# Optimization experiments

Hardware: AMD Instinct MI355X
Metric: run time of the kernel (lower is better)

The kernel has to match this reference:

```python
import jax, jax.numpy as jnp
import numpy as np

B, L, SIZE, ATT, LIN = 8, 2048, 1024, 1024, 4096
EPS = 1e-5


def layer_norm(x, g, b):
    m = x.mean(-1, keepdims=True)
    v = ((x - m) ** 2).mean(-1, keepdims=True)
    return (x - m) * jax.lax.rsqrt(v + EPS) * g + b


def time_shift(x):
    # ZeroPad2d((0,0,1,-1)): prepend a zero timestep, drop the last one
    return jnp.pad(x, ((0, 0), (1, 0), (0, 0)))[:, :-1]


def wkv(time_decay, time_first, k, v):
    """RWKV-v4 WKV linear-attention recurrence (numerically stable, log-space max tracking).
    k, v: (B, L, D). Returns (B, L, D)."""
    w = -jnp.exp(time_decay)  # (D,) per-channel decay (negative)
    u = time_first            # (D,) bonus for current token

    def step(carry, kv):
        p, q, o = carry  # numerator, denominator, running max exponent: (B, D)
        kt, vt = kv      # (B, D)
        no = jnp.maximum(o, u + kt)
        A = jnp.exp(o - no)
        Bc = jnp.exp(u + kt - no)
        out = (A * p + Bc * vt) / (A * q + Bc)
        no2 = jnp.maximum(o + w, kt)
        A2 = jnp.exp(o + w - no2)
        B2 = jnp.exp(kt - no2)
        return (A2 * p + B2 * vt, A2 * q + B2, no2), out

    Bn, Ln, D = k.shape
    init = (jnp.zeros((Bn, D), k.dtype), jnp.zeros((Bn, D), k.dtype),
            jnp.full((Bn, D), -1e38, k.dtype))
    _, out = jax.lax.scan(step, init, (jnp.moveaxis(k, 1, 0), jnp.moveaxis(v, 1, 0)))
    return jnp.moveaxis(out, 0, 1)


def setup_inputs() -> dict:
    key = jax.random.key(0)
    ks = jax.random.split(key, 20)
    n = lambda i, shape, s=1.0: jax.random.normal(ks[i], shape, jnp.float32) * s
    u = lambda i, shape: jax.random.uniform(ks[i], shape, jnp.float32)
    return {
        "x": n(0, (B, L, SIZE)),
        "ln_att_g": jnp.ones((SIZE,), jnp.float32), "ln_att_b": jnp.zeros((SIZE,), jnp.float32),
        "ln_ffn_g": jnp.ones((SIZE,), jnp.float32), "ln_ffn_b": jnp.zeros((SIZE,), jnp.float32),
        "att_time_decay": n(1, (ATT,), 0.5), "att_time_first": n(2, (ATT,), 0.5),
        "att_mix_k": u(3, (SIZE,)), "att_mix_v": u(4, (SIZE,)), "att_mix_r": u(5, (SIZE,)),
        "att_wk": n(6, (SIZE, ATT), 0.02), "att_wv": n(7, (SIZE, ATT), 0.02),
        "att_wr": n(8, (SIZE, ATT), 0.02), "att_wo": n(9, (ATT, SIZE), 0.02),
        "ffn_mix_k": u(10, (SIZE,)), "ffn_mix_r": u(11, (SIZE,)),
        "ffn_wk": n(12, (SIZE, LIN), 0.02), "ffn_wv": n(13, (LIN, SIZE), 0.02),
        "ffn_wr": n(14, (SIZE, SIZE), 0.02),
    }


def reference(x, ln_att_g, ln_att_b, ln_ffn_g, ln_ffn_b,
              att_time_decay, att_time_first, att_mix_k, att_mix_v, att_mix_r,
              att_wk, att_wv, att_wr, att_wo,
              ffn_mix_k, ffn_mix_r, ffn_wk, ffn_wv, ffn_wr):
    # --- time-mixing (WKV attention) branch ---
    h = layer_norm(x, ln_att_g, ln_att_b)
    sx = time_shift(h)
    k = (h * att_mix_k + sx * (1.0 - att_mix_k)) @ att_wk
    v = (h * att_mix_v + sx * (1.0 - att_mix_v)) @ att_wv
    r = jax.nn.sigmoid((h * att_mix_r + sx * (1.0 - att_mix_r)) @ att_wr)
    att = (r * wkv(att_time_decay, att_time_first, k, v)) @ att_wo
    x = x + att  # dropout rate 0.0 (eval)
    # --- channel-mixing (FFN) branch ---
    h = layer_norm(x, ln_ffn_g, ln_ffn_b)
    sx = time_shift(h)
    kf = jnp.square(jax.nn.relu((h * ffn_mix_k + sx * (1.0 - ffn_mix_k)) @ ffn_wk))
    rf = jax.nn.sigmoid((h * ffn_mix_r + sx * (1.0 - ffn_mix_r)) @ ffn_wr)
    return x + rf * (kf @ ffn_wv)
```

## Files before the change

### kernel.cpp

```cpp
#include <hip/hip_runtime.h>
#include <cstdint>
#include <cstddef>

#define BB   8
#define LLEN 2048
#define DSZ  1024
#define FFN  4096
#define MROWS (BB*LLEN)
#define EPSLN 1e-5f
#define WKV_C 64
#define WKV_S (LLEN/WKV_C)
#define WKV_STATES (BB*WKV_C*DSZ)

typedef __bf16 bh8 __attribute__((ext_vector_type(8)));
typedef float  f32x4 __attribute__((ext_vector_type(4)));

__device__ __forceinline__ unsigned short f32_to_bf16(float f) {
  unsigned int u = __float_as_uint(f);
  u += 0x7FFFu + ((u >> 16) & 1u);
  return (unsigned short)(u >> 16);
}
__device__ __forceinline__ float bf16_to_f32(unsigned short u) {
  return __uint_as_float(((unsigned int)u) << 16);
}
__device__ __forceinline__ float bf16_lo(unsigned int u) {
  return __uint_as_float(u << 16);
}
__device__ __forceinline__ float bf16_hi(unsigned int u) {
  return __uint_as_float(u & 0xFFFF0000u);
}
__device__ __forceinline__ unsigned int pack_bf16(float lo, float hi) {
  return (unsigned int)f32_to_bf16(lo) | ((unsigned int)f32_to_bf16(hi) << 16);
}
__device__ __forceinline__ float fexp(float x) { return __expf(x); }
__device__ __forceinline__ float frcp(float x) { return __builtin_amdgcn_rcpf(x); }

__device__ __forceinline__ void load_lds16(const void* g, void* l) {
  __builtin_amdgcn_global_load_lds((const __attribute__((address_space(1))) void*)g,
                                   (__attribute__((address_space(3))) void*)l, 16, 0, 0);
}

#define RAW_BAR() asm volatile("s_barrier" ::: "memory")
#define WAIT_VM4() asm volatile("s_waitcnt vmcnt(4)" ::: "memory")
#define WAIT_VM0() asm volatile("s_waitcnt vmcnt(0)" ::: "memory")

struct TD { const float* s; unsigned short* d; int K; int N; };
struct TDs { TD t[7]; int base[8]; };

__global__ __launch_bounds__(256) void transpose_all(TDs td) {
  __shared__ float tile[32][33];
  int bid = blockIdx.x;
  int i = 0;
#pragma unroll
  for (int j = 1; j < 7; ++j) if (bid >= td.base[j]) i = j;
  const float* W = td.t[i].s;
  unsigned short* Wt = td.t[i].d;
  int K = td.t[i].K, N = td.t[i].N;
  int lid = bid - td.base[i];
  int gx = N >> 5;
  int n0 = (lid % gx) * 32, k0 = (lid / gx) * 32;
  int tx = threadIdx.x & 31, ty = threadIdx.x >> 5;
#pragma unroll
  for (int j = 0; j < 32; j += 8)
    tile[ty + j][tx] = W[(size_t)(k0 + ty + j) * N + n0 + tx];
  __syncthreads();
#pragma unroll
  for (int j = 0; j < 32; j += 8)
    Wt[(size_t)(n0 + ty + j) * K + k0 + tx] = f32_to_bf16(tile[tx][ty + j]);
}

__global__ __launch_bounds__(256) void lnmix_att(const float* __restrict__ x,
                                                 const float* __restrict__ g,
                                                 const float* __restrict__ bb,
                                                 const float* __restrict__ mk,
                                                 const float* __restrict__ mv,
                                                 const float* __restrict__ mr,
                                                 unsigned short* __restrict__ xk,
                                                 unsigned short* __restrict__ xv,
                                                 unsigned short* __restrict__ xr) {
  int row = blockIdx.x;
  int t = row & (LLEN - 1);
  int tid = threadIdx.x;
  float4 vc = ((const float4*)(x + (size_t)row * DSZ))[tid];
  float4 vp = make_float4(0.f, 0.f, 0.f, 0.f);
  if (t > 0) vp = ((const float4*)(x + (size_t)(row - 1) * DSZ))[tid];
  float sc = vc.x + vc.y + vc.z + vc.w;
  float qc = vc.x * vc.x + vc.y * vc.y + vc.z * vc.z + vc.w * vc.w;
  float sp = vp.x + vp.y + vp.z + vp.w;
  float qp = vp.x * vp.x + vp.y * vp.y + vp.z * vp.z + vp.w * vp.w;
#pragma unroll
  for (int off = 32; off; off >>= 1) {
    sc += __shfl_down(sc, off); qc += __shfl_down(qc, off);
    sp += __shfl_down(sp, off); qp += __shfl_down(qp, off);
  }
  __shared__ float red[16];
  int lane = tid & 63, w = tid >> 6;
  if (lane == 0) { red[w] = sc; red[4 + w] = qc; red[8 + w] = sp; red[12 + w] = qp; }
  __syncthreads();
  if (tid < 4) red[tid * 4] = red[tid * 4] + red[tid * 4 + 1] + red[tid * 4 + 2] + red[tid * 4 + 3];
  __syncthreads();
  const float invD = 1.f / DSZ;
  float mc = red[0] * invD, rc = rsqrtf(red[4] * invD - mc * mc + EPSLN);
  float mp = red[8] * invD, rp = rsqrtf(red[12] * invD - mp * mp + EPSLN);
  float4 G = ((const float4*)g)[tid], Bv = ((const float4*)bb)[tid];
  float c[4] = { vc.x, vc.y, vc.z, vc.w };
  float p[4] = { vp.x, vp.y, vp.z, vp.w };
  float Ga[4] = { G.x, G.y, G.z, G.w };
  float Ba[4] = { Bv.x, Bv.y, Bv.z, Bv.w };
  float4 K = ((const float4*)mk)[tid];
  float4 V = ((const float4*)mv)[tid];
  float4 R = ((const float4*)mr)[tid];
  float Ka[4] = { K.x, K.y, K.z, K.w };
  float Va[4] = { V.x, V.y, V.z, V.w };
  float Ra[4] = { R.x, R.y, R.z, R.w };
  ushort4 ok, ov, orr;
  unsigned short* okp = &ok.x; unsigned short* ovp = &ov.x; unsigned short* orp = &orr.x;
#pragma unroll
  for (int e = 0; e < 4; ++e) {
    float hc = (c[e] - mc) * rc * Ga[e] + Ba[e];
    float hp = (t > 0) ? (p[e] - mp) * rp * Ga[e] + Ba[e] : 0.f;
    okp[e] = f32_to_bf16(hc * Ka[e] + hp * (1.f - Ka[e]));
    ovp[e] = f32_to_bf16(hc * Va[e] + hp * (1.f - Va[e]));
    orp[e] = f32_to_bf16(hc * Ra[e] + hp * (1.f - Ra[e]));
  }
  size_t e4 = (size_t)row * DSZ + tid * 4;
  *(ushort4*)(xk + e4) = ok;
  *(ushort4*)(xv + e4) = ov;
  *(ushort4*)(xr + e4) = orr;
}

__global__ __launch_bounds__(256) void lnmix_ffn(const float* __restrict__ x,
                                                 const float* __restrict__ g,
                                                 const float* __restrict__ bb,
                                                 const float* __restrict__ mk,
                                                 const float* __restrict__ mr,
                                                 unsigned short* __restrict__ xk,
                                                 unsigned short* __restrict__ xr) {
  int row = blockIdx.x;
  int t = row & (LLEN - 1);
  int tid = threadIdx.x;
  float4 vc = ((const float4*)(x + (size_t)row * DSZ))[tid];
  float4 vp = make_float4(0.f, 0.f, 0.f, 0.f);
  if (t > 0) vp = ((const float4*)(x + (size_t)(row - 1) * DSZ))[tid];
  float sc = vc.x + vc.y + vc.z + vc.w;
  float qc = vc.x * vc.x + vc.y * vc.y + vc.z * vc.z + vc.w * vc.w;
  float sp = vp.x + vp.y + vp.z + vp.w;
  float qp = vp.x * vp.x + vp.y * vp.y + vp.z * vp.z + vp.w * vp.w;
#pragma unroll
  for (int off = 32; off; off >>= 1) {
    sc += __shfl_down(sc, off); qc += __shfl_down(qc, off);
    sp += __shfl_down(sp, off); qp += __shfl_down(qp, off);
  }
  __shared__ float red[16];
  int lane = tid & 63, w = tid >> 6;
  if (lane == 0) { red[w] = sc; red[4 + w] = qc; red[8 + w] = sp; red[12 + w] = qp; }
  __syncthreads();
  if (tid < 4) red[tid * 4] = red[tid * 4] + red[tid * 4 + 1] + red[tid * 4 + 2] + red[tid * 4 + 3];
  __syncthreads();
  const float invD = 1.f / DSZ;
  float mc = red[0] * invD, rc = rsqrtf(red[4] * invD - mc * mc + EPSLN);
  float mp = red[8] * invD, rp = rsqrtf(red[12] * invD - mp * mp + EPSLN);
  float4 G = ((const float4*)g)[tid], Bv = ((const float4*)bb)[tid];
  float c[4] = { vc.x, vc.y, vc.z, vc.w };
  float p[4] = { vp.x, vp.y, vp.z, vp.w };
  float Ga[4] = { G.x, G.y, G.z, G.w };
  float Ba[4] = { Bv.x, Bv.y, Bv.z, Bv.w };
  float4 K = ((const float4*)mk)[tid];
  float4 R = ((const float4*)mr)[tid];
  float Ka[4] = { K.x, K.y, K.z, K.w };
  float Ra[4] = { R.x, R.y, R.z, R.w };
  ushort4 ok, orr;
  unsigned short* okp = &ok.x; unsigned short* orp = &orr.x;
#pragma unroll
  for (int e = 0; e < 4; ++e) {
    float hc = (c[e] - mc) * rc * Ga[e] + Ba[e];
    float hp = (t > 0) ? (p[e] - mp) * rp * Ga[e] + Ba[e] : 0.f;
    okp[e] = f32_to_bf16(hc * Ka[e] + hp * (1.f - Ka[e]));
    orp[e] = f32_to_bf16(hc * Ra[e] + hp * (1.f - Ra[e]));
  }
  size_t e4 = (size_t)row * DSZ + tid * 4;
  *(ushort4*)(xk + e4) = ok;
  *(ushort4*)(xr + e4) = orr;
}

__global__ __launch_bounds__(256) void wkv_pass1(const unsigned int* __restrict__ kk2,
                                                 const unsigned int* __restrict__ vv2,
                                                 const float* __restrict__ td,
                                                 float* __restrict__ sP,
                                                 float* __restrict__ sQ,
                                                 float* __restrict__ sO) {
  int gid = blockIdx.x * 256 + threadIdx.x;
  int d2 = gid & 511;
  int bc = gid >> 9;
  int c  = bc & (WKV_C - 1);
  int b  = bc >> 6;
  int d0 = d2 * 2;
  float w0 = -fexp(td[d0]), w1 = -fexp(td[d0 + 1]);
  size_t base = ((size_t)b * LLEN + (size_t)c * WKV_S) * 512 + d2;
  float p0 = 0.f, q0 = 0.f, o0 = -1e38f;
  float p1 = 0.f, q1 = 0.f, o1 = -1e38f;
  unsigned int kc = kk2[base], vc = vv2[base];
  unsigned int kA = 0, vA = 0, kB = 0, vB = 0;
  if (WKV_S > 1) { kA = kk2[base + 512]; vA = vv2[base + 512]; }
  for (int t = 0; t < WKV_S; ++t) {
    if (t + 2 < WKV_S) {
      size_t nxt = base + (size_t)(t + 2) * 512;
      kB = kk2[nxt]; vB = vv2[nxt];
    } else { kB = 0; vB = 0; }
    {
      float kt = bf16_lo(kc), vt = bf16_lo(vc);
      float ow = o0 + w0;
      float no2 = fmaxf(ow, kt);
      float A2 = fexp(ow - no2), B2 = fexp(kt - no2);
      p0 = A2 * p0 + B2 * vt; q0 = A2 * q0 + B2; o0 = no2;
    }
    {
      float kt = bf16_hi(kc), vt = bf16_hi(vc);
      float ow = o1 + w1;
      float no2 = fmaxf(ow, kt);
      float A2 = fexp(ow - no2), B2 = fexp(kt - no2);
      p1 = A2 * p1 + B2 * vt; q1 = A2 * q1 + B2; o1 = no2;
    }
    kc = kA; vc = vA; kA = kB; vA = vB;
  }
  int sidx = (bc << 10) + d0;
  sP[sidx] = p0; sP[sidx + 1] = p1;
  sQ[sidx] = q0; sQ[sidx + 1] = q1;
  sO[sidx] = o0; sO[sidx + 1] = o1;
}

__global__ __launch_bounds__(256) void wkv_combine(const float* __restrict__ sP,
                                                   const float* __restrict__ sQ,
                                                   const float* __restrict__ sO,
                                                   const float* __restrict__ td,
                                                   float* __restrict__ pP,
                                                   float* __restrict__ pQ,
                                                   float* __restrict__ pO) {
  int gid = blockIdx.x * 256 + threadIdx.x;
  int d = gid & (DSZ - 1);
  int b = gid >> 10;
  float w = -fexp(td[d]);
  float Sw = (float)WKV_S * w;
  float p = 0.f, q = 0.f, o = -1e38f;
  for (int c = 0; c < WKV_C; ++c) {
    size_t idx = (((size_t)b * WKV_C + c) << 10) + d;
    pP[idx] = p; pQ[idx] = q; pO[idx] = o;
    float lp = sP[idx], lq = sQ[idx], lo = sO[idx];
    float oin = o + Sw;
    float no  = fmaxf(oin, lo);
    float Ai  = fexp(oin - no);
    float Al  = fexp(lo - no);
    p = Ai * p + Al * lp;
    q = Ai * q + Al * lq;
    o = no;
  }
}

__global__ __launch_bounds__(256) void wkv_pass3(const unsigned int* __restrict__ kk2,
                                                 const unsigned int* __restrict__ vv2,
                                                 const unsigned int* __restrict__ rr2,
                                                 const float* __restrict__ td,
                                                 const float* __restrict__ tf,
                                                 const float* __restrict__ pP,
                                                 const float* __restrict__ pQ,
                                                 const float* __restrict__ pO,
                                                 unsigned int* __restrict__ rw2) {
  int gid = blockIdx.x * 256 + threadIdx.x;
  int d2 = gid & 511;
  int bc = gid >> 9;
  int c  = bc & (WKV_C - 1);
  int b  = bc >> 6;
  int d0 = d2 * 2;
  float w0 = -fexp(td[d0]), w1 = -fexp(td[d0 + 1]);
  float u0 = tf[d0], u1 = tf[d0 + 1];
  int sidx = (bc << 10) + d0;
  float p0 = pP[sidx], q0 = pQ[sidx], o0 = pO[sidx];
  float p1 = pP[sidx + 1], q1 = pQ[sidx + 1], o1 = pO[sidx + 1];
  size_t base = ((size_t)b * LLEN + (size_t)c * WKV_S) * 512 + d2;
  unsigned int kc = kk2[base], vc = vv2[base], rc = rr2[base];
  unsigned int kA = 0, vA = 0, rA = 0, kB = 0, vB = 0, rB = 0;
  if (WKV_S > 1) { kA = kk2[base + 512]; vA = vv2[base + 512]; rA = rr2[base + 512]; }
  for (int t = 0; t < WKV_S; ++t) {
    if (t + 2 < WKV_S) {
      size_t nxt = base + (size_t)(t + 2) * 512;
      kB = kk2[nxt]; vB = vv2[nxt]; rB = rr2[nxt];
    } else { kB = 0; vB = 0; rB = 0; }
    float out0, out1;
    {
      float kt = bf16_lo(kc), vt = bf16_lo(vc);
      float uk = u0 + kt;
      float no = fmaxf(o0, uk);
      float A  = fexp(o0 - no), Bc = fexp(uk - no);
      out0 = (A * p0 + Bc * vt) * frcp(A * q0 + Bc);
      float ow = o0 + w0;
      float no2 = fmaxf(ow, kt);
      float A2 = fexp(ow - no2), B2 = fexp(kt - no2);
      p0 = A2 * p0 + B2 * vt; q0 = A2 * q0 + B2; o0 = no2;
    }
    {
      float kt = bf16_hi(kc), vt = bf16_hi(vc);
      float uk = u1 + kt;
      float no = fmaxf(o1, uk);
      float A  = fexp(o1 - no), Bc = fexp(uk - no);
      out1 = (A * p1 + Bc * vt) * frcp(A * q1 + Bc);
      float ow = o1 + w1;
      float no2 = fmaxf(ow, kt);
      float A2 = fexp(ow - no2), B2 = fexp(kt - no2);
      p1 = A2 * p1 + B2 * vt; q1 = A2 * q1 + B2; o1 = no2;
    }
    rw2[base + (size_t)t * 512] = pack_bf16(bf16_lo(rc) * out0, bf16_hi(rc) * out1);
    kc = kA; vc = vA; rc = rA; kA = kB; vA = vB; rA = rB;
  }
}

#define KTILE_BODY(T)                                                             \
  {                                                                               \
    const int buf  = ((T) & 1) << 15;                                             \
    const int bufn = buf ^ 32768;                                                 \
    bh8 a03[4][2], a47[4][2], b01[2][2], b23[2][2];                               \
                                                           \
    _Pragma("unroll")                                                             \
    for (int mi = 0; mi < 4; ++mi) {                                              \
      a03[mi][0] = *(const bh8*)(smA + buf + aRow + mi * 2048 + sw0);             \
      a03[mi][1] = *(const bh8*)(smA + buf + aRow + mi * 2048 + sw1);             \
    }                                                                             \
    _Pragma("unroll")                                                             \
    for (int nj = 0; nj < 2; ++nj) {                                              \
      b01[nj][0] = *(const bh8*)(smB + buf + bRow + nj * 2048 + sw0);             \
      b01[nj][1] = *(const bh8*)(smB + buf + bRow + nj * 2048 + sw1);             \
    }                                                                             \
    _Pragma("unroll")                                                             \
    for (int nj = 0; nj < 2; ++nj) {                                              \
      b23[nj][0] = *(const bh8*)(smB + buf + bRow + (nj + 2) * 2048 + sw0);       \
      b23[nj][1] = *(const bh8*)(smB + buf + bRow + (nj + 2) * 2048 + sw1);       \
    }                                                                             \
    if ((T) + 1 < nk) {                                                           \
      load_lds16(pA0  + 64, smA + bufn + ldsW);                                   \
      load_lds16(pA0b + 64, smA + bufn + 1024 + ldsW);                            \
      load_lds16(pA1  + 64, smA + bufn + 16384 + ldsW);                           \
      load_lds16(pA1b + 64, smA + bufn + 16384 + 1024 + ldsW);                    \
    }                                                                             \
    __builtin_amdgcn_s_setprio(1);                                                \
    _Pragma("unroll")                                                             \
    for (int mi = 0; mi < 4; ++mi)                                                \
      _Pragma("unroll")                                                           \
      for (int nj = 0; nj < 2; ++nj) {                                            \
        acc[mi][nj] = __builtin_amdgcn_mfma_f32_16x16x32_bf16(a03[mi][0], b01[nj][0], acc[mi][nj], 0, 0, 0); \
        acc[mi][nj] = __builtin_amdgcn_mfma_f32_16x16x32_bf16(a03[mi][1], b01[nj][1], acc[mi][nj], 0, 0, 0); \
      }                                                                           \
    _Pragma("unroll")                                                             \
    for (int mi = 0; mi < 4; ++mi)                                                \
      _Pragma("unroll")                                                           \
      for (int nj = 0; nj < 2; ++nj) {                                            \
        acc[mi][nj + 2] = __builtin_amdgcn_mfma_f32_16x16x32_bf16(a03[mi][0], b23[nj][0], acc[mi][nj + 2], 0, 0, 0); \
        acc[mi][nj + 2] = __builtin_amdgcn_mfma_f32_16x16x32_bf16(a03[mi][1], b23[nj][1], acc[mi][nj + 2], 0, 0, 0); \
      }                                                                           \
    __builtin_amdgcn_s_setprio(0);                                                \
    RAW_BAR();                                                                    \
                                                           \
    _Pragma("unroll")                                                             \
    for (int mi = 0; mi < 4; ++mi) {                                              \
      a47[mi][0] = *(const bh8*)(smA + buf + aRow + (mi + 4) * 2048 + sw0);       \
      a47[mi][1] = *(const bh8*)(smA + buf + aRow + (mi + 4) * 2048 + sw1);       \
    }                                                                             \
    if ((T) + 2 < nk) {                                                           \
      load_lds16(pB0  + 128, smB + buf + ldsW);                                   \
      load_lds16(pB0b + 128, smB + buf + 1024 + ldsW);                            \
      load_lds16(pB1  + 128, smB + buf + 16384 + ldsW);                           \
      load_lds16(pB1b + 128, smB + buf + 16384 + 1024 + ldsW);                    \
    }                                                                             \
    __builtin_amdgcn_s_setprio(1);                                                \
    _Pragma("unroll")                                                             \
    for (int mi = 0; mi < 4; ++mi)                                                \
      _Pragma("unroll")                                                           \
      for (int nj = 0; nj < 2; ++nj) {                                            \
        acc[mi + 4][nj] = __builtin_amdgcn_mfma_f32_16x16x32_bf16(a47[mi][0], b01[nj][0], acc[mi + 4][nj], 0, 0, 0); \
        acc[mi + 4][nj] = __builtin_amdgcn_mfma_f32_16x16x32_bf16(a47[mi][1], b01[nj][1], acc[mi + 4][nj], 0, 0, 0); \
      }                                                                           \
    _Pragma("unroll")                                                             \
    for (int mi = 0; mi < 4; ++mi)                                                \
      _Pragma("unroll")                                                           \
      for (int nj = 0; nj < 2; ++nj) {                                            \
        acc[mi + 4][nj + 2] = __builtin_amdgcn_mfma_f32_16x16x32_bf16(a47[mi][0], b23[nj][0], acc[mi + 4][nj + 2], 0, 0, 0); \
        acc[mi + 4][nj + 2] = __builtin_amdgcn_mfma_f32_16x16x32_bf16(a47[mi][1], b23[nj][1], acc[mi + 4][nj + 2], 0, 0, 0); \
      }                                                                           \
    __builtin_amdgcn_s_setprio(0);                                                \
    if ((T) + 2 < nk) { WAIT_VM4(); } else { WAIT_VM0(); }                        \
    RAW_BAR();                                                                    \
  }

#define GEMM_SETUP(AB, BB_, KD)                                                   \
  const unsigned short* Ab = (AB);                                                \
  const unsigned short* Bb = (BB_);                                               \
  const int nk = (KD) >> 6;                                                       \
  const int r15 = lane & 15;                                                      \
  const int sw0 = ((((lane >> 4)    ) ^ (lane & 7)) << 4);                        \
  const int sw1 = (((4 | (lane >> 4)) ^ (lane & 7)) << 4);                        \
  const int aRow = wr * 16384 + r15 * 128;                                        \
  const int bRow = wc * 8192  + r15 * 128;                                        \
  const int ldsW = wid * 2048 + lane * 16;                                        \
  const int grow = lane >> 3;                                                     \
  const int colS = (((lane & 7) ^ grow) << 3);                                    \
  const unsigned short* pA0  = Ab + (size_t)(wid * 16 + grow) * (KD) + colS;      \
  const unsigned short* pA0b = pA0 + (size_t)8 * (KD);                            \
  const unsigned short* pA1  = pA0 + (size_t)128 * (KD);                          \
  const unsigned short* pA1b = pA1 + (size_t)8 * (KD);                            \
  const unsigned short* pB0  = Bb + (size_t)(wid * 16 + grow) * (KD) + colS;      \
  const unsigned short* pB0b = pB0 + (size_t)8 * (KD);                            \
  const unsigned short* pB1  = pB0 + (size_t)128 * (KD);                          \
  const unsigned short* pB1b = pB1 + (size_t)8 * (KD);                            \
  f32x4 acc[8][4];                                                                \
  _Pragma("unroll")                                                               \
  for (int i = 0; i < 8; ++i)                                                     \
    _Pragma("unroll")                                                             \
    for (int j = 0; j < 4; ++j)                                                   \
      _Pragma("unroll")                                                           \
      for (int e = 0; e < 4; ++e) acc[i][j][e] = 0.f;                             \
        \
  load_lds16(pA0,       smA + ldsW);                                              \
  load_lds16(pA0b,      smA + 1024 + ldsW);                                       \
  load_lds16(pA1,       smA + 16384 + ldsW);                                      \
  load_lds16(pA1b,      smA + 16384 + 1024 + ldsW);                               \
  load_lds16(pB0,       smB + ldsW);                                              \
  load_lds16(pB0b,      smB + 1024 + ldsW);                                       \
  load_lds16(pB1,       smB + 16384 + ldsW);                                      \
  load_lds16(pB1b,      smB + 16384 + 1024 + ldsW);                               \
  if (nk > 1) {                                                                   \
    load_lds16(pB0  + 64, smB + 32768 + ldsW);                                    \
    load_lds16(pB0b + 64, smB + 32768 + 1024 + ldsW);                             \
    load_lds16(pB1  + 64, smB + 32768 + 16384 + ldsW);                            \
    load_lds16(pB1b + 64, smB + 32768 + 16384 + 1024 + ldsW);                     \
    WAIT_VM4();                                                                   \
  } else {                                                                        \
    WAIT_VM0();                                                                   \
  }                                                                               \
  RAW_BAR();                                                                      \
  for (int tb = 0; tb < nk; ++tb) {                                               \
    KTILE_BODY(tb)                                                                \
    pA0 += 64; pA0b += 64; pA1 += 64; pA1b += 64;                                 \
    pB0 += 64; pB0b += 64; pB1 += 64; pB1b += 64;                                 \
  }

template <int EPI>
__global__ __launch_bounds__(512, 1) void gemm256(const unsigned short* __restrict__ A,
                                                  const unsigned short* __restrict__ Bt,
                                                  float* __restrict__ C,
                                                  unsigned short* __restrict__ Cbf,
                                                  const float* __restrict__ aux1,
                                                  const unsigned short* __restrict__ aux2b,
                                                  int M, int N, int K) {
  extern __shared__ unsigned char sm[];
  unsigned char* smA = sm;
  unsigned char* smB = sm + 65536;
  const int tid  = threadIdx.x;
  const int lane = tid & 63;
  const int wid  = tid >> 6;
  const int wr   = wid >> 2;
  const int wc   = wid & 3;
  int nwg = gridDim.x;
  int gx  = N >> 8;
  int wg  = blockIdx.x;
  int swzid = ((nwg & 7) == 0) ? ((wg & 7) * (nwg >> 3) + (wg >> 3)) : wg;
  int bn = swzid % gx, bm = swzid / gx;

  GEMM_SETUP(A + (size_t)bm * 256 * K, Bt + (size_t)bn * 256 * K, K)

  const int r4 = (lane >> 4) * 4, cn = lane & 15;
#pragma unroll
  for (int mi = 0; mi < 8; ++mi) {
#pragma unroll
    for (int nj = 0; nj < 4; ++nj) {
      int col = bn * 256 + wc * 64 + nj * 16 + cn;
#pragma unroll
      for (int e = 0; e < 4; ++e) {
        int row = bm * 256 + wr * 128 + mi * 16 + r4 + e;
        size_t idx = (size_t)row * N + col;
        float val = acc[mi][nj][e];
        if (EPI == 0) {
          Cbf[idx] = f32_to_bf16(val);
        } else if (EPI == 1) {
          Cbf[idx] = f32_to_bf16(frcp(1.f + fexp(-val)));
        } else if (EPI == 2) {
          C[idx] = aux1[idx] + val;
        } else if (EPI == 3) {
          float tt = val > 0.f ? val : 0.f;
          Cbf[idx] = f32_to_bf16(tt * tt);
        } else {
          C[idx] = aux1[idx] + bf16_to_f32(aux2b[idx]) * val;
        }
      }
    }
  }
}

__global__ __launch_bounds__(512, 1) void gemm256_kvr(const unsigned short* __restrict__ A0,
                                                      const unsigned short* __restrict__ A1,
                                                      const unsigned short* __restrict__ A2,
                                                      const unsigned short* __restrict__ B0w,
                                                      const unsigned short* __restrict__ B1w,
                                                      const unsigned short* __restrict__ B2w,
                                                      unsigned short* __restrict__ D0,
                                                      unsigned short* __restrict__ D1,
                                                      unsigned short* __restrict__ D2) {
  extern __shared__ unsigned char sm[];
  unsigned char* smA = sm;
  unsigned char* smB = sm + 65536;
  const int tid  = threadIdx.x;
  const int lane = tid & 63;
  const int wid  = tid >> 6;
  const int wr   = wid >> 2;
  const int wc   = wid & 3;
  int nwg = gridDim.x;
  int wg  = blockIdx.x;
  int swzid = (wg & 7) * (nwg >> 3) + (wg >> 3);
  int gsel  = swzid >> 8;
  int local = swzid & 255;
  int bn = local & 3, bm = local >> 2;

  const unsigned short* Asel = (gsel == 0) ? A0 : (gsel == 1) ? A1 : A2;
  const unsigned short* Bsel = (gsel == 0) ? B0w : (gsel == 1) ? B1w : B2w;
  unsigned short*       Dsel = (gsel == 0) ? D0 : (gsel == 1) ? D1 : D2;

  GEMM_SETUP(Asel + (size_t)bm * 256 * DSZ, Bsel + (size_t)bn * 256 * DSZ, DSZ)

  const int r4 = (lane >> 4) * 4, cn = lane & 15;
  const bool sig = (gsel == 2);
#pragma unroll
  for (int mi = 0; mi < 8; ++mi) {
#pragma unroll
    for (int nj = 0; nj < 4; ++nj) {
      int col = bn * 256 + wc * 64 + nj * 16 + cn;
#pragma unroll
      for (int e = 0; e < 4; ++e) {
        int row = bm * 256 + wr * 128 + mi * 16 + r4 + e;
        size_t idx = (size_t)row * DSZ + col;
        float val = acc[mi][nj][e];
        Dsel[idx] = f32_to_bf16(sig ? frcp(1.f + fexp(-val)) : val);
      }
    }
  }
}

extern "C" void kernel_launch(void* const* d_in, const int* in_sizes, int n_in,
                              void* d_out, int out_size, void* d_ws, size_t ws_size,
                              hipStream_t stream) {
  const float* x        = (const float*)d_in[0];
  const float* ln_att_g = (const float*)d_in[1];
  const float* ln_att_b = (const float*)d_in[2];
  const float* ln_ffn_g = (const float*)d_in[3];
  const float* ln_ffn_b = (const float*)d_in[4];
  const float* td       = (const float*)d_in[5];
  const float* tf       = (const float*)d_in[6];
  const float* amk      = (const float*)d_in[7];
  const float* amv      = (const float*)d_in[8];
  const float* amr      = (const float*)d_in[9];
  const float* att_wk   = (const float*)d_in[10];
  const float* att_wv   = (const float*)d_in[11];
  const float* att_wr   = (const float*)d_in[12];
  const float* att_wo   = (const float*)d_in[13];
  const float* fmk      = (const float*)d_in[14];
  const float* fmr      = (const float*)d_in[15];
  const float* ffn_wk   = (const float*)d_in[16];
  const float* ffn_wv   = (const float*)d_in[17];
  const float* ffn_wr   = (const float*)d_in[18];
  float* out = (float*)d_out;
  (void)in_sizes; (void)n_in; (void)out_size;

  const size_t WBYTES  = 4 * ((size_t)DSZ * DSZ * 2)
                       + (size_t)FFN * DSZ * 2
                       + (size_t)DSZ * FFN * 2
                       + (size_t)DSZ * DSZ * 2;
  const size_t BUF     = (size_t)MROWS * DSZ * 2;
  const size_t NEEDED  = WBYTES + 4 * BUF + 2 * BUF;
  if (ws_size < NEEDED) return;

  char* ws = (char*)d_ws;
  size_t off = 0;
  auto take = [&](size_t bytes) { char* p = ws + off; off += (bytes + 255) & ~(size_t)255; return p; };

  unsigned short* wkT  = (unsigned short*)take((size_t)DSZ * DSZ * 2);
  unsigned short* wvT  = (unsigned short*)take((size_t)DSZ * DSZ * 2);
  unsigned short* wrT  = (unsigned short*)take((size_t)DSZ * DSZ * 2);
  unsigned short* woT  = (unsigned short*)take((size_t)DSZ * DSZ * 2);
  unsigned short* fwkT = (unsigned short*)take((size_t)FFN * DSZ * 2);
  unsigned short* fwvT = (unsigned short*)take((size_t)DSZ * FFN * 2);
  unsigned short* fwrT = (unsigned short*)take((size_t)DSZ * DSZ * 2);
  unsigned short* bufA = (unsigned short*)take(BUF);
  unsigned short* bufB = (unsigned short*)take(BUF);
  unsigned short* bufC = (unsigned short*)take(BUF);
  unsigned short* bufD = (unsigned short*)take(BUF);
  char*           eReg = take(2 * BUF);
  unsigned short* kf = bufC;
  unsigned short* vBuf = (unsigned short*)eReg;
  unsigned short* rBuf = (unsigned short*)(eReg + BUF);

  float* sP = (float*)bufA;
  float* sQ = sP + WKV_STATES;
  float* sO = sQ + WKV_STATES;
  float* pP = sO + WKV_STATES;
  float* pQ = pP + WKV_STATES;
  float* pO = pQ + WKV_STATES;

  TDs tds;
  tds.t[0] = { att_wk, wkT,  DSZ, DSZ };
  tds.t[1] = { att_wv, wvT,  DSZ, DSZ };
  tds.t[2] = { att_wr, wrT,  DSZ, DSZ };
  tds.t[3] = { att_wo, woT,  DSZ, DSZ };
  tds.t[4] = { ffn_wr, fwrT, DSZ, DSZ };
  tds.t[5] = { ffn_wk, fwkT, DSZ, FFN };
  tds.t[6] = { ffn_wv, fwvT, FFN, DSZ };
  int acc = 0;
  for (int i = 0; i < 7; ++i) {
    tds.base[i] = acc;
    acc += (tds.t[i].N >> 5) * (tds.t[i].K >> 5);
  }
  tds.base[7] = acc;
  transpose_all<<<acc, 256, 0, stream>>>(tds);

  const int LDSB = 131072;
  const int G1   = (MROWS / 256) * (DSZ / 256);
  const int G2   = (MROWS / 256) * (FFN / 256);

  lnmix_att<<<MROWS, 256, 0, stream>>>(x, ln_att_g, ln_att_b, amk, amv, amr, bufA, bufB, bufC);
  gemm256_kvr<<<3 * G1, 512, LDSB, stream>>>(bufA, bufB, bufC, wkT, wvT, wrT, bufD, vBuf, rBuf);
  wkv_pass1<<<(WKV_STATES / 2) / 256, 256, 0, stream>>>((const unsigned int*)bufD, (const unsigned int*)vBuf, td, sP, sQ, sO);
  wkv_combine<<<(BB * DSZ) / 256, 256, 0, stream>>>(sP, sQ, sO, td, pP, pQ, pO);
  wkv_pass3<<<(WKV_STATES / 2) / 256, 256, 0, stream>>>((const unsigned int*)bufD, (const unsigned int*)vBuf, (const unsigned int*)rBuf, td, tf, pP, pQ, pO, (unsigned int*)bufB);
  gemm256<2><<<G1, 512, LDSB, stream>>>(bufB, woT, out, nullptr, x, nullptr, MROWS, DSZ, DSZ);

  lnmix_ffn<<<MROWS, 256, 0, stream>>>(out, ln_ffn_g, ln_ffn_b, fmk, fmr, bufA, bufB);
  gemm256<3><<<G2, 512, LDSB, stream>>>(bufA, fwkT, nullptr, kf, nullptr, nullptr, MROWS, FFN, DSZ);
  gemm256<1><<<G1, 512, LDSB, stream>>>(bufB, fwrT, nullptr, bufA, nullptr, nullptr, MROWS, DSZ, DSZ);
  gemm256<4><<<G1, 512, LDSB, stream>>>(kf, fwvT, out, nullptr, out, bufA, MROWS, DSZ, FFN);
}
```

Measured before the change: 613.1 us.

## Merge transpose with attention layernorm and fold WKV chunk combine into pass3

Measured after the change: 613.5 us. About the same (+0.1%).

```diff
diff --git a/kernel.cpp b/kernel.cpp
--- a/kernel.cpp
+++ b/kernel.cpp
@@ -11,6 +11,7 @@
 #define WKV_C 64
 #define WKV_S (LLEN/WKV_C)
 #define WKV_STATES (BB*WKV_C*DSZ)
+#define NTRANS 13312
 
 typedef __bf16 bh8 __attribute__((ext_vector_type(8)));
 typedef float  f32x4 __attribute__((ext_vector_type(4)));
@@ -47,38 +48,40 @@
 struct TD { const float* s; unsigned short* d; int K; int N; };
 struct TDs { TD t[7]; int base[8]; };
 
-__global__ __launch_bounds__(256) void transpose_all(TDs td) {
+__global__ __launch_bounds__(256) void prelude(TDs td,
+                                               const float* __restrict__ x,
+                                               const float* __restrict__ g,
+                                               const float* __restrict__ bb,
+                                               const float* __restrict__ mk,
+                                               const float* __restrict__ mv,
+                                               const float* __restrict__ mr,
+                                               unsigned short* __restrict__ xk,
+                                               unsigned short* __restrict__ xv,
+                                               unsigned short* __restrict__ xr) {
   __shared__ float tile[32][33];
+  __shared__ float red[16];
   int bid = blockIdx.x;
-  int i = 0;
-#pragma unroll
-  for (int j = 1; j < 7; ++j) if (bid >= td.base[j]) i = j;
-  const float* W = td.t[i].s;
-  unsigned short* Wt = td.t[i].d;
-  int K = td.t[i].K, N = td.t[i].N;
-  int lid = bid - td.base[i];
-  int gx = N >> 5;
-  int n0 = (lid % gx) * 32, k0 = (lid / gx) * 32;
-  int tx = threadIdx.x & 31, ty = threadIdx.x >> 5;
-#pragma unroll
-  for (int j = 0; j < 32; j += 8)
-    tile[ty + j][tx] = W[(size_t)(k0 + ty + j) * N + n0 + tx];
-  __syncthreads();
-#pragma unroll
-  for (int j = 0; j < 32; j += 8)
-    Wt[(size_t)(n0 + ty + j) * K + k0 + tx] = f32_to_bf16(tile[tx][ty + j]);
-}
-
-__global__ __launch_bounds__(256) void lnmix_att(const float* __restrict__ x,
-                                                 const float* __restrict__ g,
-                                                 const float* __restrict__ bb,
-                                                 const float* __restrict__ mk,
-                                                 const float* __restrict__ mv,
-                                                 const float* __restrict__ mr,
-                                                 unsigned short* __restrict__ xk,
-                                                 unsigned short* __restrict__ xv,
-                                                 unsigned short* __restrict__ xr) {
-  int row = blockIdx.x;
+  if (bid < NTRANS) {
+    int i = 0;
+#pragma unroll
+    for (int j = 1; j < 7; ++j) if (bid >= td.base[j]) i = j;
+    const float* W = td.t[i].s;
+    unsigned short* Wt = td.t[i].d;
+    int K = td.t[i].K, N = td.t[i].N;
+    int lid = bid - td.base[i];
+    int gx = N >> 5;
+    int n0 = (lid % gx) * 32, k0 = (lid / gx) * 32;
+    int tx = threadIdx.x & 31, ty = threadIdx.x >> 5;
+#pragma unroll
+    for (int j = 0; j < 32; j += 8)
+      tile[ty + j][tx] = W[(size_t)(k0 + ty + j) * N + n0 + tx];
+    __syncthreads();
+#pragma unroll
+    for (int j = 0; j < 32; j += 8)
+      Wt[(size_t)(n0 + ty + j) * K + k0 + tx] = f32_to_bf16(tile[tx][ty + j]);
+    return;
+  }
+  int row = bid - NTRANS;
   int t = row & (LLEN - 1);
   int tid = threadIdx.x;
   float4 vc = ((const float4*)(x + (size_t)row * DSZ))[tid];
@@ -93,7 +96,6 @@
     sc += __shfl_down(sc, off); qc += __shfl_down(qc, off);
     sp += __shfl_down(sp, off); qp += __shfl_down(qp, off);
   }
-  __shared__ float red[16];
   int lane = tid & 63, w = tid >> 6;
   if (lane == 0) { red[w] = sc; red[4 + w] = qc; red[8 + w] = sp; red[12 + w] = qp; }
   __syncthreads();
@@ -229,41 +231,14 @@
   sO[sidx] = o0; sO[sidx + 1] = o1;
 }
 
-__global__ __launch_bounds__(256) void wkv_combine(const float* __restrict__ sP,
-                                                   const float* __restrict__ sQ,
-                                                   const float* __restrict__ sO,
-                                                   const float* __restrict__ td,
-                                                   float* __restrict__ pP,
-                                                   float* __restrict__ pQ,
-                                                   float* __restrict__ pO) {
-  int gid = blockIdx.x * 256 + threadIdx.x;
-  int d = gid & (DSZ - 1);
-  int b = gid >> 10;
-  float w = -fexp(td[d]);
-  float Sw = (float)WKV_S * w;
-  float p = 0.f, q = 0.f, o = -1e38f;
-  for (int c = 0; c < WKV_C; ++c) {
-    size_t idx = (((size_t)b * WKV_C + c) << 10) + d;
-    pP[idx] = p; pQ[idx] = q; pO[idx] = o;
-    float lp = sP[idx], lq = sQ[idx], lo = sO[idx];
-    float oin = o + Sw;
-    float no  = fmaxf(oin, lo);
-    float Ai  = fexp(oin - no);
-    float Al  = fexp(lo - no);
-    p = Ai * p + Al * lp;
-    q = Ai * q + Al * lq;
-    o = no;
-  }
-}
-
 __global__ __launch_bounds__(256) void wkv_pass3(const unsigned int* __restrict__ kk2,
                                                  const unsigned int* __restrict__ vv2,
                                                  const unsigned int* __restrict__ rr2,
                                                  const float* __restrict__ td,
                                                  const float* __restrict__ tf,
-                                                 const float* __restrict__ pP,
-                                                 const float* __restrict__ pQ,
-                                                 const float* __restrict__ pO,
+                                                 const float* __restrict__ sP,
+                                                 const float* __restrict__ sQ,
+                                                 const float* __restrict__ sO,
                                                  unsigned int* __restrict__ rw2) {
   int gid = blockIdx.x * 256 + threadIdx.x;
   int d2 = gid & 511;
@@ -273,9 +248,23 @@
   int d0 = d2 * 2;
   float w0 = -fexp(td[d0]), w1 = -fexp(td[d0 + 1]);
   float u0 = tf[d0], u1 = tf[d0 + 1];
-  int sidx = (bc << 10) + d0;
-  float p0 = pP[sidx], q0 = pQ[sidx], o0 = pO[sidx];
-  float p1 = pP[sidx + 1], q1 = pQ[sidx + 1], o1 = pO[sidx + 1];
+  float Sw0 = (float)WKV_S * w0, Sw1 = (float)WKV_S * w1;
+  float p0 = 0.f, q0 = 0.f, o0 = -1e38f;
+  float p1 = 0.f, q1 = 0.f, o1 = -1e38f;
+  int cbase = (b * WKV_C) << 10;
+  for (int cc = 0; cc < c; ++cc) {
+    int idx = cbase + (cc << 10) + d0;
+    float lp0 = sP[idx],     lq0 = sQ[idx],     lo0 = sO[idx];
+    float lp1 = sP[idx + 1], lq1 = sQ[idx + 1], lo1 = sO[idx + 1];
+    float oin0 = o0 + Sw0;
+    float no0  = fmaxf(oin0, lo0);
+    float Ai0  = fexp(oin0 - no0), Al0 = fexp(lo0 - no0);
+    p0 = Ai0 * p0 + Al0 * lp0; q0 = Ai0 * q0 + Al0 * lq0; o0 = no0;
+    float oin1 = o1 + Sw1;
+    float no1  = fmaxf(oin1, lo1);
+    float Ai1  = fexp(oin1 - no1), Al1 = fexp(lo1 - no1);
+    p1 = Ai1 * p1 + Al1 * lp1; q1 = Ai1 * q1 + Al1 * lq1; o1 = no1;
+  }
   size_t base = ((size_t)b * LLEN + (size_t)c * WKV_S) * 512 + d2;
   unsigned int kc = kk2[base], vc = vv2[base], rc = rr2[base];
   unsigned int kA = 0, vA = 0, rA = 0, kB = 0, vB = 0, rB = 0;
@@ -597,9 +586,6 @@
   float* sP = (float*)bufA;
   float* sQ = sP + WKV_STATES;
   float* sO = sQ + WKV_STATES;
-  float* pP = sO + WKV_STATES;
-  float* pQ = pP + WKV_STATES;
-  float* pO = pQ + WKV_STATES;
 
   TDs tds;
   tds.t[0] = { att_wk, wkT,  DSZ, DSZ };
@@ -615,17 +601,16 @@
     acc += (tds.t[i].N >> 5) * (tds.t[i].K >> 5);
   }
   tds.base[7] = acc;
-  transpose_all<<<acc, 256, 0, stream>>>(tds);
+  prelude<<<NTRANS + MROWS, 256, 0, stream>>>(tds, x, ln_att_g, ln_att_b,
+                                              amk, amv, amr, bufA, bufB, bufC);
 
   const int LDSB = 131072;
   const int G1   = (MROWS / 256) * (DSZ / 256);
   const int G2   = (MROWS / 256) * (FFN / 256);
 
-  lnmix_att<<<MROWS, 256, 0, stream>>>(x, ln_att_g, ln_att_b, amk, amv, amr, bufA, bufB, bufC);
   gemm256_kvr<<<3 * G1, 512, LDSB, stream>>>(bufA, bufB, bufC, wkT, wvT, wrT, bufD, vBuf, rBuf);
   wkv_pass1<<<(WKV_STATES / 2) / 256, 256, 0, stream>>>((const unsigned int*)bufD, (const unsigned int*)vBuf, td, sP, sQ, sO);
-  wkv_combine<<<(BB * DSZ) / 256, 256, 0, stream>>>(sP, sQ, sO, td, pP, pQ, pO);
-  wkv_pass3<<<(WKV_STATES / 2) / 256, 256, 0, stream>>>((const unsigned int*)bufD, (const unsigned int*)vBuf, (const unsigned int*)rBuf, td, tf, pP, pQ, pO, (unsigned int*)bufB);
+  wkv_pass3<<<(WKV_STATES / 2) / 256, 256, 0, stream>>>((const unsigned int*)bufD, (const unsigned int*)vBuf, (const unsigned int*)rBuf, td, tf, sP, sQ, sO, (unsigned int*)bufB);
   gemm256<2><<<G1, 512, LDSB, stream>>>(bufB, woT, out, nullptr, x, nullptr, MROWS, DSZ, DSZ);
 
   lnmix_ffn<<<MROWS, 256, 0, stream>>>(out, ln_ffn_g, ln_ffn_b, fmk, fmr, bufA, bufB);
```
